# Kernel optimization log

Hardware: AMD Instinct MI355X
Metric: run time of the kernel (lower is better)

## Reference

```python
import jax, jax.numpy as jnp
import numpy as np

T, D = 1024, 2048
H, KH, HD = 16, 4, 128
E, K, I = 8, 2, 2048
EPS = 1e-5
CAP = 30.0          # attn logit softcap and router logit softcap
BASE = 10000.0      # rope theta


def setup_inputs() -> dict:
    key = jax.random.key(0)
    ks = jax.random.split(key, 8)
    s = 0.02
    return {
        "positions": jnp.arange(T, dtype=jnp.int32),
        "hidden_states": jax.random.normal(ks[0], (T, D), jnp.float32),
        "w_qkv": jax.random.normal(ks[1], (D, (H + 2 * KH) * HD), jnp.float32) * s,
        "w_o": jax.random.normal(ks[2], (H * HD, D), jnp.float32) * s,
        "w_gate": jax.random.normal(ks[3], (D, E), jnp.float32) * s,
        "w_gate_up": jax.random.normal(ks[4], (E, D, 2 * I), jnp.float32) * s,
        "w_down": jax.random.normal(ks[5], (E, I, D), jnp.float32) * s,
        "w_pre_attn": 1.0 + 0.01 * jax.random.normal(ks[6], (D,), jnp.float32),
        "w_post_attn": jnp.ones((D,), jnp.float32),
        "w_pre_moe": 1.0 + 0.01 * jax.random.normal(ks[7], (D,), jnp.float32),
        "w_post_moe": jnp.ones((D,), jnp.float32),
    }


def rmsnorm(x, w):
    v = jnp.mean(jnp.square(x), axis=-1, keepdims=True)
    return x * jax.lax.rsqrt(v + EPS) * w


def rope_neox(pos, x):
    # x: [T, nH, HD]; full-head-dim neox-style rotation
    half = HD // 2
    inv = 1.0 / (BASE ** (jnp.arange(half, dtype=jnp.float32) * 2.0 / HD))
    f = pos.astype(jnp.float32)[:, None] * inv            # [T, half]
    cos, sin = jnp.cos(f)[:, None, :], jnp.sin(f)[:, None, :]
    x1, x2 = x[..., :half], x[..., half:]
    return jnp.concatenate([x1 * cos - x2 * sin, x2 * cos + x1 * sin], axis=-1)


def attention(pos, x, w_qkv, w_o):
    qkv = x @ w_qkv
    q, k, v = jnp.split(qkv, [H * HD, (H + KH) * HD], axis=-1)
    q = rope_neox(pos, q.reshape(T, H, HD))
    k = rope_neox(pos, k.reshape(T, KH, HD))
    v = v.reshape(T, KH, HD)
    rep = H // KH                                          # GQA repeat
    k = jnp.repeat(k, rep, axis=1)
    v = jnp.repeat(v, rep, axis=1)
    s = jnp.einsum('qhd,khd->hqk', q, k) * (HD ** -0.5)
    s = CAP * jnp.tanh(s / CAP)                            # tanh logit cap
    causal = pos[:, None] >= pos[None, :]
    s = jnp.where(causal[None], s, -1e30)
    p = jax.nn.softmax(s, axis=-1)
    o = jnp.einsum('hqk,khd->qhd', p, v).reshape(T, H * HD)
    return o @ w_o


def moe(x, w_gate, w_gate_up, w_down):
    logits = x @ w_gate
    logits = CAP * jnp.tanh(logits / CAP)                  # router softcap
    probs = jax.nn.softmax(logits, axis=-1)
    topv, topi = jax.lax.top_k(probs, K)                   # no renorm (Grok1)
    comb = jnp.zeros((T, E), probs.dtype).at[jnp.arange(T)[:, None], topi].set(topv)
    gu = jnp.einsum('td,edf->etf', x, w_gate_up)           # [E,T,2I]
    g, u = jnp.split(gu, 2, axis=-1)
    act = jax.nn.gelu(g, approximate=True) * u             # GeluAndMul(tanh)
    out_e = jnp.einsum('eti,eid->etd', act, w_down)        # [E,T,D]
    return jnp.einsum('etd,te->td', out_e, comb)


def reference(positions, hidden_states, w_qkv, w_o, w_gate, w_gate_up, w_down,
              w_pre_attn, w_post_attn, w_pre_moe, w_post_moe):
    resid = hidden_states
    h = rmsnorm(hidden_states, w_pre_attn)
    a = attention(positions, h, w_qkv, w_o)
    resid = resid + rmsnorm(a, w_post_attn)                # post_attn_norm + add
    h = rmsnorm(resid, w_pre_moe)
    m = moe(h, w_gate, w_gate_up, w_down)
    return resid + rmsnorm(m, w_post_moe)
```

## Files before the change

### kernel.cpp

```cpp
#include <hip/hip_runtime.h>

#define TT 1024
#define DD 2048
#define NH 16
#define NKV 4
#define HDIM 128
#define NE 8
#define NI 2048
#define EPSF 1e-5f

typedef short bf16x8 __attribute__((ext_vector_type(8)));
typedef float f32x4 __attribute__((ext_vector_type(4)));

__device__ __forceinline__ unsigned short f2bf(float x) {
  unsigned u = __float_as_uint(x);
  u += 0x7FFFu + ((u >> 16) & 1u);
  return (unsigned short)(u >> 16);
}
__device__ __forceinline__ float bf2f(unsigned short h) {
  return __uint_as_float((unsigned)h << 16);
}
__device__ __forceinline__ void split2(float a, unsigned short& h,
                                       unsigned short& l) {
  h = f2bf(a);
  l = f2bf(a - bf2f(h));
}

__device__ __forceinline__ float wave_sum(float v) {
#pragma unroll
  for (int m = 32; m >= 1; m >>= 1) v += __shfl_xor(v, m, 64);
  return v;
}
__device__ __forceinline__ float wave_max(float v) {
#pragma unroll
  for (int m = 32; m >= 1; m >>= 1) v = fmaxf(v, __shfl_xor(v, m, 64));
  return v;
}

__device__ __forceinline__ int swz4(int r) { return (r ^ (r >> 2)) & 3; }
__device__ __forceinline__ int swz8(int r) { return (r ^ (r >> 3)) & 7; }

__device__ __forceinline__ void stage32(char* dst, const unsigned short* src,
                                        int rs, int tid) {
#pragma unroll
  for (int j = 0; j < 2; ++j) {
    int idx = tid + j * 256;
    int r = idx >> 2, c = idx & 3;
    bf16x8 v = *(const bf16x8*)(src + r * rs + c * 8);
    *(bf16x8*)(dst + r * 64 + ((c ^ swz4(r)) << 4)) = v;
  }
}
__device__ __forceinline__ void ld_frag(const char* base, int wrow, int l15,
                                        int lg, bf16x8* dst) {
#pragma unroll
  for (int i = 0; i < 4; ++i) {
    int row = wrow + i * 16 + l15;
    dst[i] = *(const bf16x8*)(base + row * 64 + ((lg ^ swz4(row)) << 4));
  }
}
__device__ __forceinline__ void mm16(const bf16x8* xa, const bf16x8* xb,
                                     f32x4 (*acc)[4]) {
#pragma unroll
  for (int mi = 0; mi < 4; ++mi)
#pragma unroll
    for (int ni = 0; ni < 4; ++ni)
      acc[mi][ni] = __builtin_amdgcn_mfma_f32_16x16x32_bf16(
          xa[mi], xb[ni], acc[mi][ni], 0, 0, 0);
}

template <int MODE>
__global__ __launch_bounds__(256) void pgemm3_k(
    const unsigned short* __restrict__ Ah, const unsigned short* __restrict__ Al,
    const unsigned short* __restrict__ Bh, const unsigned short* __restrict__ Bl,
    float* __restrict__ C, int Kh, int lda, int ldb, int ldc, long czs,
    float escale) {
  int z = blockIdx.z;
  int m0 = blockIdx.y * 128, n0 = blockIdx.x * 128;
  int k0 = 0, kend = Kh;
  if (MODE == 0) {
    k0 = z * Kh;
    kend = k0 + Kh;
    C += (long)z * czs;
  } else if (MODE == 1) {
    if (blockIdx.x > blockIdx.y) return;
    Ah += (long)z * TT * lda;
    Al += (long)z * TT * lda;
    Bh += (long)(z >> 2) * TT * ldb;
    Bl += (long)(z >> 2) * TT * ldb;
    C += (long)z * czs;
  } else {
    int head = z >> 2, ch = z & 3;
    int limit = (blockIdx.y + 1) * 128;
    k0 = ch * 256;
    if (k0 >= limit) return;
    kend = k0 + 256 < limit ? k0 + 256 : limit;
    Ah += (long)head * TT * lda;
    Al += (long)head * TT * lda;
    Bh += (long)(head >> 2) * HDIM * ldb;
    Bl += (long)(head >> 2) * HDIM * ldb;
    C += (long)ch * czs + head * HDIM;
  }

  __shared__ __align__(16) char lds[32768];
  int tid = threadIdx.x, lane = tid & 63, wid = tid >> 6;
  int wm = (wid >> 1) * 64, wn = (wid & 1) * 64;
  int l15 = lane & 15, lg = lane >> 4;

  f32x4 acc[4][4];
#pragma unroll
  for (int i = 0; i < 4; ++i)
#pragma unroll
    for (int j = 0; j < 4; ++j) acc[i][j] = {0.f, 0.f, 0.f, 0.f};

  for (int kt = k0; kt < kend; kt += 32) {
    __syncthreads();
    stage32(lds, Ah + (long)m0 * lda + kt, lda, tid);
    stage32(lds + 8192, Al + (long)m0 * lda + kt, lda, tid);
    stage32(lds + 16384, Bh + (long)n0 * ldb + kt, ldb, tid);
    stage32(lds + 24576, Bl + (long)n0 * ldb + kt, ldb, tid);
    __syncthreads();
    bf16x8 fah[4], fal[4], fbh[4], fbl[4];
    ld_frag(lds, wm, l15, lg, fah);
    ld_frag(lds + 16384, wn, l15, lg, fbh);
    mm16(fah, fbh, acc);
    ld_frag(lds + 24576, wn, l15, lg, fbl);
    mm16(fah, fbl, acc);
    ld_frag(lds + 8192, wm, l15, lg, fal);
    mm16(fal, fbh, acc);
  }
#pragma unroll
  for (int mi = 0; mi < 4; ++mi)
#pragma unroll
    for (int ni = 0; ni < 4; ++ni)
#pragma unroll
      for (int rr = 0; rr < 4; ++rr) {
        int ml = m0 + wm + mi * 16 + lg * 4 + rr;
        int col = n0 + wn + ni * 16 + l15;
        float val = acc[mi][ni][rr];
        if (MODE == 1) {
          val *= escale;
          val = 30.f * tanhf(val * (1.f / 30.f));
        }
        C[(long)ml * ldc + col] = val;
      }
}

template <int AMODE, int EP>
__global__ __launch_bounds__(256) void gemm_k(
    const unsigned short* __restrict__ A, const float* __restrict__ Bf,
    float* __restrict__ Cf, int N, int K, int lda, int ldb, int ldc, long bzs,
    const int* __restrict__ cnt, const int* __restrict__ basep,
    const int* __restrict__ tok, const int* __restrict__ slotp,
    const float* __restrict__ wtp, float* __restrict__ slots_out) {
  int z = blockIdx.z;
  Bf += (long)z * bzs;
  int Me = cnt[z], be = basep[z];
  int m0 = blockIdx.y * 128, n0 = blockIdx.x * 128;
  if (m0 >= Me) return;

  __shared__ __align__(16) char lds[32768];
  const int BOFF = 16384;
  int tid = threadIdx.x, lane = tid & 63, wid = tid >> 6;
  int wm = (wid >> 1) * 64, wn = (wid & 1) * 64;
  int l15 = lane & 15, lg = lane >> 4;

  f32x4 acc[4][4];
#pragma unroll
  for (int i = 0; i < 4; ++i)
#pragma unroll
    for (int j = 0; j < 4; ++j) acc[i][j] = {0.f, 0.f, 0.f, 0.f};

  for (int kt = 0; kt < K; kt += 64) {
    __syncthreads();
#pragma unroll
    for (int i = 0; i < 4; ++i) {
      int idx = tid + i * 256;
      int r = idx >> 3, c = idx & 7;
      int gm = m0 + r;
      bf16x8 v = {0, 0, 0, 0, 0, 0, 0, 0};
      bool ok = gm < Me;
      long arow;
      if (AMODE == 1)
        arow = ok ? (long)tok[z * TT + gm] : 0;
      else
        arow = (long)be + gm;
      if (ok) v = *(const bf16x8*)(A + arow * (long)lda + kt + c * 8);
      *(bf16x8*)(lds + r * 128 + ((c ^ swz8(r)) << 4)) = v;
    }
#pragma unroll
    for (int i = 0; i < 4; ++i) {
      int gidx = tid + i * 256;
      int n = gidx & 127, kc = gidx >> 7;
      const float* src = Bf + (long)(kt + kc * 8) * ldb + n0 + n;
      bf16x8 v;
#pragma unroll
      for (int u = 0; u < 8; ++u)
        ((unsigned short*)&v)[u] = f2bf(src[(long)u * ldb]);
      *(bf16x8*)(lds + BOFF + n * 128 + ((kc ^ swz8(n)) << 4)) = v;
    }
    __syncthreads();
#pragma unroll
    for (int s = 0; s < 2; ++s) {
      bf16x8 af[4], bfr[4];
      int slotk = s * 4 + lg;
#pragma unroll
      for (int mi = 0; mi < 4; ++mi) {
        int row = wm + mi * 16 + l15;
        af[mi] =
            *(const bf16x8*)(lds + row * 128 + ((slotk ^ swz8(row)) << 4));
      }
#pragma unroll
      for (int ni = 0; ni < 4; ++ni) {
        int row = wn + ni * 16 + l15;
        bfr[ni] = *(const bf16x8*)(lds + BOFF + row * 128 +
                                   ((slotk ^ swz8(row)) << 4));
      }
      mm16(af, bfr, acc);
    }
  }
#pragma unroll
  for (int mi = 0; mi < 4; ++mi)
#pragma unroll
    for (int ni = 0; ni < 4; ++ni)
#pragma unroll
      for (int rr = 0; rr < 4; ++rr) {
        int ml = m0 + wm + mi * 16 + lg * 4 + rr;
        int col = n0 + wn + ni * 16 + l15;
        float val = acc[mi][ni][rr];
        if (ml < Me) {
          if (EP == 0) {
            Cf[(long)(be + ml) * ldc + col] = val;
          } else {
            int t = tok[z * TT + ml];
            int s = slotp[z * TT + ml];
            float w = wtp[z * TT + ml];
            slots_out[((long)s * TT + t) * DD + col] = val * w;
          }
        }
      }
}

__global__ __launch_bounds__(256) void tsplit_k(const float* __restrict__ W,
                                                unsigned short* __restrict__ Th,
                                                unsigned short* __restrict__ Tl,
                                                int K, int N) {
  __shared__ float lds[64 * 65];
  int n0 = blockIdx.x * 64, k0 = blockIdx.y * 64;
  int tid = threadIdx.x;
#pragma unroll
  for (int i = 0; i < 4; ++i) {
    int idx = tid + i * 256;
    int kr = idx >> 4, cg = idx & 15;
    float4 v = *(const float4*)(W + (long)(k0 + kr) * N + n0 + cg * 4);
    float* p = &lds[kr * 65 + cg * 4];
    p[0] = v.x; p[1] = v.y; p[2] = v.z; p[3] = v.w;
  }
  __syncthreads();
#pragma unroll
  for (int i = 0; i < 2; ++i) {
    int idx = tid + i * 256;
    int n = idx >> 3, kc = idx & 7;
    bf16x8 h8, l8;
#pragma unroll
    for (int u = 0; u < 8; ++u) {
      unsigned short hh, ll;
      split2(lds[(kc * 8 + u) * 65 + n], hh, ll);
      ((unsigned short*)&h8)[u] = hh;
      ((unsigned short*)&l8)[u] = ll;
    }
    long o = (long)(n0 + n) * K + k0 + kc * 8;
    *(bf16x8*)(Th + o) = h8;
    *(bf16x8*)(Tl + o) = l8;
  }
}

__global__ __launch_bounds__(256) void rms_pre_k(const float* __restrict__ x,
                                                 const float* __restrict__ w,
                                                 unsigned short* __restrict__ oh,
                                                 unsigned short* __restrict__ ol) {
  __shared__ float red[4];
  int t = blockIdx.x, tid = threadIdx.x;
  const float* xr = x + (long)t * DD;
  float xv[8];
  float ss = 0.f;
#pragma unroll
  for (int i = 0; i < 8; ++i) {
    float v = xr[tid + i * 256];
    xv[i] = v;
    ss += v * v;
  }
  ss = wave_sum(ss);
  if ((tid & 63) == 0) red[tid >> 6] = ss;
  __syncthreads();
  float r = rsqrtf((red[0] + red[1] + red[2] + red[3]) * (1.f / DD) + EPSF);
#pragma unroll
  for (int i = 0; i < 8; ++i) {
    int d = tid + i * 256;
    split2(xv[i] * r * w[d], oh[(long)t * DD + d], ol[(long)t * DD + d]);
  }
}

__global__ __launch_bounds__(256) void rope_qk_k(
    const int* __restrict__ pos, const float* __restrict__ p0,
    const float* __restrict__ p1, unsigned short* __restrict__ qh,
    unsigned short* __restrict__ ql, unsigned short* __restrict__ kh,
    unsigned short* __restrict__ kl) {
  __shared__ float cs[64], sn[64];
  int t = blockIdx.x, tid = threadIdx.x;
  float pf = (float)pos[t];
  if (tid < 64) {
    float inv = exp2f(-(float)tid * 0.20762050593046015f);
    float f = pf * inv;
    cs[tid] = cosf(f);
    sn[tid] = sinf(f);
  }
  __syncthreads();
  const float* r0 = p0 + (long)t * 3072;
  const float* r1 = p1 + (long)t * 3072;
#pragma unroll
  for (int i = 0; i < 4; ++i) {
    int idx = tid + i * 256;
    int h = idx >> 6, j = idx & 63;
    float x1 = r0[h * HDIM + j] + r1[h * HDIM + j];
    float x2 = r0[h * HDIM + 64 + j] + r1[h * HDIM + 64 + j];
    float c = cs[j], s = sn[j];
    long base = ((long)h * TT + t) * HDIM;
    split2(x1 * c - x2 * s, qh[base + j], ql[base + j]);
    split2(x2 * c + x1 * s, qh[base + 64 + j], ql[base + 64 + j]);
  }
  {
    int k2 = tid >> 6, j = tid & 63;
    float x1 = r0[2048 + k2 * HDIM + j] + r1[2048 + k2 * HDIM + j];
    float x2 = r0[2048 + k2 * HDIM + 64 + j] + r1[2048 + k2 * HDIM + 64 + j];
    float c = cs[j], s = sn[j];
    long base = ((long)k2 * TT + t) * HDIM;
    split2(x1 * c - x2 * s, kh[base + j], kl[base + j]);
    split2(x2 * c + x1 * s, kh[base + 64 + j], kl[base + 64 + j]);
  }
}

__global__ __launch_bounds__(256) void vtrans_k(const float* __restrict__ p0,
                                                const float* __restrict__ p1,
                                                unsigned short* __restrict__ Vh,
                                                unsigned short* __restrict__ Vl) {
  __shared__ float lds[64 * 129];
  int tb = blockIdx.x, kv = blockIdx.y;
  int t0 = tb * 128;
  int tid = threadIdx.x;
#pragma unroll
  for (int dh = 0; dh < 2; ++dh) {
    if (dh) __syncthreads();
#pragma unroll
    for (int i = 0; i < 8; ++i) {
      int fidx = tid + i * 256;
      int t = fidx >> 4, dq = fidx & 15;
      long gi = (long)(t0 + t) * 3072 + 2560 + kv * HDIM + dh * 64 + dq * 4;
      float4 a = *(const float4*)(p0 + gi);
      float4 b = *(const float4*)(p1 + gi);
      lds[(dq * 4 + 0) * 129 + t] = a.x + b.x;
      lds[(dq * 4 + 1) * 129 + t] = a.y + b.y;
      lds[(dq * 4 + 2) * 129 + t] = a.z + b.z;
      lds[(dq * 4 + 3) * 129 + t] = a.w + b.w;
    }
    __syncthreads();
#pragma unroll
    for (int i = 0; i < 4; ++i) {
      int cidx = tid + i * 256;
      int d = cidx >> 4, tc = cidx & 15;
      bf16x8 h8, l8;
#pragma unroll
      for (int u = 0; u < 8; ++u) {
        unsigned short hh, ll;
        split2(lds[d * 129 + tc * 8 + u], hh, ll);
        ((unsigned short*)&h8)[u] = hh;
        ((unsigned short*)&l8)[u] = ll;
      }
      long o = ((long)kv * HDIM + dh * 64 + d) * TT + t0 + tc * 8;
      *(bf16x8*)(Vh + o) = h8;
      *(bf16x8*)(Vl + o) = l8;
    }
  }
}

__global__ __launch_bounds__(256) void softmax_k(const float* __restrict__ S,
                                                 unsigned short* __restrict__ Ph,
                                                 unsigned short* __restrict__ Pl) {
  __shared__ float red[4];
  int i = blockIdx.x, h = blockIdx.y, tid = threadIdx.x;
  int len = i + 1;
  const float* srow = S + ((long)h * TT + i) * TT;
  unsigned short* ph = Ph + ((long)h * TT + i) * TT;
  unsigned short* pl = Pl + ((long)h * TT + i) * TT;
  float m = -1e30f;
  for (int j = tid; j < len; j += 256) m = fmaxf(m, srow[j]);
  m = wave_max(m);
  if ((tid & 63) == 0) red[tid >> 6] = m;
  __syncthreads();
  m = fmaxf(fmaxf(red[0], red[1]), fmaxf(red[2], red[3]));
  __syncthreads();
  float ssum = 0.f;
  for (int j = tid; j < len; j += 256) ssum += expf(srow[j] - m);
  ssum = wave_sum(ssum);
  if ((tid & 63) == 0) red[tid >> 6] = ssum;
  __syncthreads();
  float inv = 1.f / (red[0] + red[1] + red[2] + red[3]);
  for (int j = tid; j < TT; j += 256) {
    float p = (j < len) ? expf(srow[j] - m) * inv : 0.f;
    unsigned short hh, ll;
    split2(p, hh, ll);
    ph[j] = hh;
    pl[j] = ll;
  }
}

__global__ __launch_bounds__(256) void obreduce_k(const float* __restrict__ obp,
                                                  unsigned short* __restrict__ oh,
                                                  unsigned short* __restrict__ ol) {
  int m = blockIdx.x, tid = threadIdx.x;
  int nv = ((m >> 7) >> 1) + 1;
#pragma unroll
  for (int i = 0; i < 8; ++i) {
    int d = tid + i * 256;
    float s = 0.f;
    for (int c = 0; c < nv; ++c) s += obp[(long)c * TT * DD + (long)m * DD + d];
    split2(s, oh[(long)m * DD + d], ol[(long)m * DD + d]);
  }
}

__global__ __launch_bounds__(256) void post_attn_k(
    const float* __restrict__ a0, const float* __restrict__ a1,
    const float* __restrict__ hidden, const float* __restrict__ w_post,
    const float* __restrict__ w_pre2, float* __restrict__ resid1,
    float* __restrict__ h2f, unsigned short* __restrict__ h2b) {
  __shared__ float red[4];
  int t = blockIdx.x, tid = threadIdx.x;
  float av[8];
  float ss = 0.f;
#pragma unroll
  for (int i = 0; i < 8; ++i) {
    long o = (long)t * DD + tid + i * 256;
    float v = a0[o] + a1[o];
    av[i] = v;
    ss += v * v;
  }
  ss = wave_sum(ss);
  if ((tid & 63) == 0) red[tid >> 6] = ss;
  __syncthreads();
  float r1 = rsqrtf((red[0] + red[1] + red[2] + red[3]) * (1.f / DD) + EPSF);
  __syncthreads();
  float rv[8];
  float ss2 = 0.f;
#pragma unroll
  for (int i = 0; i < 8; ++i) {
    int d = tid + i * 256;
    float v = hidden[(long)t * DD + d] + av[i] * r1 * w_post[d];
    rv[i] = v;
    resid1[(long)t * DD + d] = v;
    ss2 += v * v;
  }
  ss2 = wave_sum(ss2);
  if ((tid & 63) == 0) red[tid >> 6] = ss2;
  __syncthreads();
  float r2 = rsqrtf((red[0] + red[1] + red[2] + red[3]) * (1.f / DD) + EPSF);
#pragma unroll
  for (int i = 0; i < 8; ++i) {
    int d = tid + i * 256;
    float hv = rv[i] * r2 * w_pre2[d];
    h2f[(long)t * DD + d] = hv;
    h2b[(long)t * DD + d] = f2bf(hv);
  }
}

__global__ __launch_bounds__(256) void gate_k(const float* __restrict__ h2f,
                                              const float* __restrict__ wg,
                                              int* cnt, int* tok, int* slotp,
                                              float* wtp) {
  __shared__ float red[4][8];
  int t = blockIdx.x, tid = threadIdx.x;
  float a[8] = {0, 0, 0, 0, 0, 0, 0, 0};
  const float* x = h2f + (long)t * DD;
  for (int d = tid; d < DD; d += 256) {
    float xv = x[d];
    const float* wr = wg + d * 8;
#pragma unroll
    for (int e = 0; e < 8; ++e) a[e] += xv * wr[e];
  }
#pragma unroll
  for (int e = 0; e < 8; ++e) a[e] = wave_sum(a[e]);
  if ((tid & 63) == 0) {
#pragma unroll
    for (int e = 0; e < 8; ++e) red[tid >> 6][e] = a[e];
  }
  __syncthreads();
  if (tid == 0) {
    float l[8], p[8];
    float m = -1e30f;
    for (int e = 0; e < 8; ++e) {
      float v = red[0][e] + red[1][e] + red[2][e] + red[3][e];
      v = 30.f * tanhf(v * (1.f / 30.f));
      l[e] = v;
      m = fmaxf(m, v);
    }
    float s = 0.f;
    for (int e = 0; e < 8; ++e) { p[e] = expf(l[e] - m); s += p[e]; }
    for (int e = 0; e < 8; ++e) p[e] /= s;
    int i1 = 0;
    for (int e = 1; e < 8; ++e) if (p[e] > p[i1]) i1 = e;
    int i2 = (i1 == 0) ? 1 : 0;
    for (int e = 0; e < 8; ++e) if (e != i1 && p[e] > p[i2]) i2 = e;
    int q1 = atomicAdd(&cnt[i1], 1);
    tok[i1 * TT + q1] = t; slotp[i1 * TT + q1] = 0; wtp[i1 * TT + q1] = p[i1];
    int q2 = atomicAdd(&cnt[i2], 1);
    tok[i2 * TT + q2] = t; slotp[i2 * TT + q2] = 1; wtp[i2 * TT + q2] = p[i2];
  }
}

__global__ void scan_k(const int* __restrict__ cnt, int* __restrict__ basep) {
  if (threadIdx.x == 0) {
    int s = 0;
    for (int e = 0; e < NE; ++e) { basep[e] = s; s += cnt[e]; }
    basep[NE] = s;
  }
}

__global__ __launch_bounds__(256) void act_k(const float* __restrict__ gu,
                                             unsigned short* __restrict__ actb) {
  long a = blockIdx.x;
  const float* g = gu + a * (2 * NI);
  for (int i = threadIdx.x; i < NI; i += 256) {
    float gg = g[i], uu = g[i + NI];
    float c = gg + 0.044715f * gg * gg * gg;
    float act = 0.5f * gg * (1.f + tanhf(0.7978845608028654f * c));
    actb[a * NI + i] = f2bf(act * uu);
  }
}

__global__ __launch_bounds__(256) void final_k(const float* __restrict__ resid1,
                                               const float* __restrict__ slots,
                                               const float* __restrict__ w2,
                                               float* __restrict__ out) {
  __shared__ float red[4];
  int t = blockIdx.x, tid = threadIdx.x;
  float mv[8];
  float ss = 0.f;
#pragma unroll
  for (int i = 0; i < 8; ++i) {
    int d = tid + i * 256;
    float v = slots[(long)t * DD + d] + slots[((long)TT + t) * DD + d];
    mv[i] = v;
    ss += v * v;
  }
  ss = wave_sum(ss);
  if ((tid & 63) == 0) red[tid >> 6] = ss;
  __syncthreads();
  float r = rsqrtf((red[0] + red[1] + red[2] + red[3]) * (1.f / DD) + EPSF);
#pragma unroll
  for (int i = 0; i < 8; ++i) {
    int d = tid + i * 256;
    out[(long)t * DD + d] = resid1[(long)t * DD + d] + mv[i] * r * w2[d];
  }
}

__global__ void sentinel_k(float* out) { out[threadIdx.x] = 12345.0f; }

extern "C" void kernel_launch(void* const* d_in, const int* in_sizes, int n_in,
                              void* d_out, int out_size, void* d_ws,
                              size_t ws_size, hipStream_t stream) {
  const int* pos = (const int*)d_in[0];
  const float* hidden = (const float*)d_in[1];
  const float* w_qkv = (const float*)d_in[2];
  const float* w_o = (const float*)d_in[3];
  const float* w_gate = (const float*)d_in[4];
  const float* w_gu = (const float*)d_in[5];
  const float* w_down = (const float*)d_in[6];
  const float* w_pre_attn = (const float*)d_in[7];
  const float* w_post_attn = (const float*)d_in[8];
  const float* w_pre_moe = (const float*)d_in[9];
  const float* w_post_moe = (const float*)d_in[10];
  float* out = (float*)d_out;

  char* ws = (char*)d_ws;
  size_t off = 0;
  auto alloc = [&](size_t bytes) {
    char* p = ws + off;
    off += (bytes + 255) & ~(size_t)255;
    return p;
  };
  typedef unsigned short u16;
  u16* h1h = (u16*)alloc((size_t)TT * DD * 2);
  u16* h1l = (u16*)alloc((size_t)TT * DD * 2);
  u16* wqkvTh = (u16*)alloc((size_t)3072 * DD * 2);
  u16* wqkvTl = (u16*)alloc((size_t)3072 * DD * 2);
  float* qkvp = (float*)alloc((size_t)2 * TT * 3072 * 4);
  u16* qh_ = (u16*)alloc((size_t)NH * TT * HDIM * 2);
  u16* ql_ = (u16*)alloc((size_t)NH * TT * HDIM * 2);
  u16* kh_ = (u16*)alloc((size_t)NKV * TT * HDIM * 2);
  u16* kl_ = (u16*)alloc((size_t)NKV * TT * HDIM * 2);
  u16* vth = (u16*)alloc((size_t)NKV * HDIM * TT * 2);
  u16* vtl = (u16*)alloc((size_t)NKV * HDIM * TT * 2);
  float* S = (float*)alloc((size_t)NH * TT * TT * 4);
  u16* Ph = (u16*)alloc((size_t)NH * TT * TT * 2);
  u16* Pl = (u16*)alloc((size_t)NH * TT * TT * 2);
  float* obp = (float*)alloc((size_t)4 * TT * DD * 4);
  u16* obh = (u16*)alloc((size_t)TT * DD * 2);
  u16* obl = (u16*)alloc((size_t)TT * DD * 2);
  u16* woTh = (u16*)alloc((size_t)DD * DD * 2);
  u16* woTl = (u16*)alloc((size_t)DD * DD * 2);
  float* attnp = (float*)alloc((size_t)2 * TT * DD * 4);
  float* resid1 = (float*)alloc((size_t)TT * DD * 4);
  float* h2f = (float*)alloc((size_t)TT * DD * 4);
  u16* h2b = (u16*)alloc((size_t)TT * DD * 2);
  int* cnt = (int*)alloc(NE * 4);
  int* basep = (int*)alloc((NE + 1) * 4);
  int* tok = (int*)alloc((size_t)NE * TT * 4);
  int* slotp = (int*)alloc((size_t)NE * TT * 4);
  float* wtp = (float*)alloc((size_t)NE * TT * 4);
  float* gu = (float*)alloc((size_t)2 * TT * 2 * NI * 4);
  u16* actb = (u16*)alloc((size_t)2 * TT * NI * 2);
  float* slots = (float*)alloc((size_t)2 * TT * DD * 4);

  if (off > ws_size) {
    sentinel_k<<<1, 256, 0, stream>>>(out);
    return;
  }

  hipMemsetAsync(cnt, 0, NE * 4, stream);
  dim3 blk(256);

  rms_pre_k<<<TT, blk, 0, stream>>>(hidden, w_pre_attn, h1h, h1l);
  tsplit_k<<<dim3(3072 / 64, DD / 64), blk, 0, stream>>>(w_qkv, wqkvTh, wqkvTl,
                                                         DD, 3072);
  tsplit_k<<<dim3(DD / 64, DD / 64), blk, 0, stream>>>(w_o, woTh, woTl, DD, DD);

  pgemm3_k<0><<<dim3(3072 / 128, TT / 128, 2), blk, 0, stream>>>(
      h1h, h1l, wqkvTh, wqkvTl, qkvp, 1024, DD, DD, 3072, (long)TT * 3072, 0.f);

  rope_qk_k<<<TT, blk, 0, stream>>>(pos, qkvp, qkvp + (size_t)TT * 3072, qh_,
                                    ql_, kh_, kl_);
  vtrans_k<<<dim3(8, NKV), blk, 0, stream>>>(qkvp, qkvp + (size_t)TT * 3072,
                                             vth, vtl);

  pgemm3_k<1><<<dim3(TT / 128, TT / 128, NH), blk, 0, stream>>>(
      qh_, ql_, kh_, kl_, S, HDIM, HDIM, HDIM, TT, (long)TT * TT,
      0.08838834764831845f);

  softmax_k<<<dim3(TT, NH), blk, 0, stream>>>(S, Ph, Pl);

  pgemm3_k<2><<<dim3(1, TT / 128, NH * 4), blk, 0, stream>>>(
      Ph, Pl, vth, vtl, obp, 256, TT, TT, DD, (long)TT * DD, 0.f);
  obreduce_k<<<TT, blk, 0, stream>>>(obp, obh, obl);

  pgemm3_k<0><<<dim3(DD / 128, TT / 128, 2), blk, 0, stream>>>(
      obh, obl, woTh, woTl, attnp, 1024, DD, DD, DD, (long)TT * DD, 0.f);

  post_attn_k<<<TT, blk, 0, stream>>>(attnp, attnp + (size_t)TT * DD, hidden,
                                      w_post_attn, w_pre_moe, resid1, h2f, h2b);
  gate_k<<<TT, blk, 0, stream>>>(h2f, w_gate, cnt, tok, slotp, wtp);
  scan_k<<<1, 64, 0, stream>>>(cnt, basep);

  gemm_k<1, 0><<<dim3(2 * NI / 128, TT / 128, NE), blk, 0, stream>>>(
      h2b, w_gu, gu, 2 * NI, DD, DD, 2 * NI, 2 * NI, (long)DD * 2 * NI, cnt,
      basep, tok, nullptr, nullptr, nullptr);

  act_k<<<2 * TT, blk, 0, stream>>>(gu, actb);

  gemm_k<2, 3><<<dim3(DD / 128, TT / 128, NE), blk, 0, stream>>>(
      actb, w_down, nullptr, DD, NI, NI, DD, DD, (long)NI * DD, cnt, basep,
      tok, slotp, wtp, slots);

  final_k<<<TT, blk, 0, stream>>>(resid1, slots, w_post_moe, out);
}
```

Measured before the change: 536.8 us.

## Split-K projections four ways, enlarge MoE GEMM tiles, trim softmax writes

```diff
diff --git a/kernel.cpp b/kernel.cpp
--- a/kernel.cpp
+++ b/kernel.cpp
@@ -8,6 +8,7 @@
 #define NE 8
 #define NI 2048
 #define EPSF 1e-5f
+#define NP 4
 
 typedef short bf16x8 __attribute__((ext_vector_type(8)));
 typedef float f32x4 __attribute__((ext_vector_type(4)));
@@ -146,7 +147,7 @@
 }
 
 template <int AMODE, int EP>
-__global__ __launch_bounds__(256) void gemm_k(
+__global__ __launch_bounds__(512) void gemm_k(
     const unsigned short* __restrict__ A, const float* __restrict__ Bf,
     float* __restrict__ Cf, int N, int K, int lda, int ldb, int ldc, long bzs,
     const int* __restrict__ cnt, const int* __restrict__ basep,
@@ -155,11 +156,11 @@
   int z = blockIdx.z;
   Bf += (long)z * bzs;
   int Me = cnt[z], be = basep[z];
-  int m0 = blockIdx.y * 128, n0 = blockIdx.x * 128;
+  int m0 = blockIdx.y * 256, n0 = blockIdx.x * 128;
   if (m0 >= Me) return;
 
-  __shared__ __align__(16) char lds[32768];
-  const int BOFF = 16384;
+  __shared__ __align__(16) char lds[49152];
+  const int BOFF = 32768;
   int tid = threadIdx.x, lane = tid & 63, wid = tid >> 6;
   int wm = (wid >> 1) * 64, wn = (wid & 1) * 64;
   int l15 = lane & 15, lg = lane >> 4;
@@ -174,7 +175,7 @@
     __syncthreads();
 #pragma unroll
     for (int i = 0; i < 4; ++i) {
-      int idx = tid + i * 256;
+      int idx = tid + i * 512;
       int r = idx >> 3, c = idx & 7;
       int gm = m0 + r;
       bf16x8 v = {0, 0, 0, 0, 0, 0, 0, 0};
@@ -188,8 +189,8 @@
       *(bf16x8*)(lds + r * 128 + ((c ^ swz8(r)) << 4)) = v;
     }
 #pragma unroll
-    for (int i = 0; i < 4; ++i) {
-      int gidx = tid + i * 256;
+    for (int i = 0; i < 2; ++i) {
+      int gidx = tid + i * 512;
       int n = gidx & 127, kc = gidx >> 7;
       const float* src = Bf + (long)(kt + kc * 8) * ldb + n0 + n;
       bf16x8 v;
@@ -301,10 +302,9 @@
 }
 
 __global__ __launch_bounds__(256) void rope_qk_k(
-    const int* __restrict__ pos, const float* __restrict__ p0,
-    const float* __restrict__ p1, unsigned short* __restrict__ qh,
-    unsigned short* __restrict__ ql, unsigned short* __restrict__ kh,
-    unsigned short* __restrict__ kl) {
+    const int* __restrict__ pos, const float* __restrict__ qp,
+    unsigned short* __restrict__ qh, unsigned short* __restrict__ ql,
+    unsigned short* __restrict__ kh, unsigned short* __restrict__ kl) {
   __shared__ float cs[64], sn[64];
   int t = blockIdx.x, tid = threadIdx.x;
   float pf = (float)pos[t];
@@ -315,14 +315,18 @@
     sn[tid] = sinf(f);
   }
   __syncthreads();
-  const float* r0 = p0 + (long)t * 3072;
-  const float* r1 = p1 + (long)t * 3072;
+  const float* row = qp + (long)t * 3072;
+  const long PS = (long)TT * 3072;
 #pragma unroll
   for (int i = 0; i < 4; ++i) {
     int idx = tid + i * 256;
     int h = idx >> 6, j = idx & 63;
-    float x1 = r0[h * HDIM + j] + r1[h * HDIM + j];
-    float x2 = r0[h * HDIM + 64 + j] + r1[h * HDIM + 64 + j];
+    float x1 = 0.f, x2 = 0.f;
+#pragma unroll
+    for (int p = 0; p < NP; ++p) {
+      x1 += row[p * PS + h * HDIM + j];
+      x2 += row[p * PS + h * HDIM + 64 + j];
+    }
     float c = cs[j], s = sn[j];
     long base = ((long)h * TT + t) * HDIM;
     split2(x1 * c - x2 * s, qh[base + j], ql[base + j]);
@@ -330,8 +334,12 @@
   }
   {
     int k2 = tid >> 6, j = tid & 63;
-    float x1 = r0[2048 + k2 * HDIM + j] + r1[2048 + k2 * HDIM + j];
-    float x2 = r0[2048 + k2 * HDIM + 64 + j] + r1[2048 + k2 * HDIM + 64 + j];
+    float x1 = 0.f, x2 = 0.f;
+#pragma unroll
+    for (int p = 0; p < NP; ++p) {
+      x1 += row[p * PS + 2048 + k2 * HDIM + j];
+      x2 += row[p * PS + 2048 + k2 * HDIM + 64 + j];
+    }
     float c = cs[j], s = sn[j];
     long base = ((long)k2 * TT + t) * HDIM;
     split2(x1 * c - x2 * s, kh[base + j], kl[base + j]);
@@ -339,14 +347,14 @@
   }
 }
 
-__global__ __launch_bounds__(256) void vtrans_k(const float* __restrict__ p0,
-                                                const float* __restrict__ p1,
+__global__ __launch_bounds__(256) void vtrans_k(const float* __restrict__ qp,
                                                 unsigned short* __restrict__ Vh,
                                                 unsigned short* __restrict__ Vl) {
   __shared__ float lds[64 * 129];
   int tb = blockIdx.x, kv = blockIdx.y;
   int t0 = tb * 128;
   int tid = threadIdx.x;
+  const long PS = (long)TT * 3072;
 #pragma unroll
   for (int dh = 0; dh < 2; ++dh) {
     if (dh) __syncthreads();
@@ -355,12 +363,16 @@
       int fidx = tid + i * 256;
       int t = fidx >> 4, dq = fidx & 15;
       long gi = (long)(t0 + t) * 3072 + 2560 + kv * HDIM + dh * 64 + dq * 4;
-      float4 a = *(const float4*)(p0 + gi);
-      float4 b = *(const float4*)(p1 + gi);
-      lds[(dq * 4 + 0) * 129 + t] = a.x + b.x;
-      lds[(dq * 4 + 1) * 129 + t] = a.y + b.y;
-      lds[(dq * 4 + 2) * 129 + t] = a.z + b.z;
-      lds[(dq * 4 + 3) * 129 + t] = a.w + b.w;
+      float4 a = *(const float4*)(qp + gi);
+#pragma unroll
+      for (int p = 1; p < NP; ++p) {
+        float4 b = *(const float4*)(qp + p * PS + gi);
+        a.x += b.x; a.y += b.y; a.z += b.z; a.w += b.w;
+      }
+      lds[(dq * 4 + 0) * 129 + t] = a.x;
+      lds[(dq * 4 + 1) * 129 + t] = a.y;
+      lds[(dq * 4 + 2) * 129 + t] = a.z;
+      lds[(dq * 4 + 3) * 129 + t] = a.w;
     }
     __syncthreads();
 #pragma unroll
@@ -388,6 +400,7 @@
   __shared__ float red[4];
   int i = blockIdx.x, h = blockIdx.y, tid = threadIdx.x;
   int len = i + 1;
+  int wlimit = ((i >> 7) + 1) << 7;
   const float* srow = S + ((long)h * TT + i) * TT;
   unsigned short* ph = Ph + ((long)h * TT + i) * TT;
   unsigned short* pl = Pl + ((long)h * TT + i) * TT;
@@ -404,7 +417,7 @@
   if ((tid & 63) == 0) red[tid >> 6] = ssum;
   __syncthreads();
   float inv = 1.f / (red[0] + red[1] + red[2] + red[3]);
-  for (int j = tid; j < TT; j += 256) {
+  for (int j = tid; j < wlimit; j += 256) {
     float p = (j < len) ? expf(srow[j] - m) * inv : 0.f;
     unsigned short hh, ll;
     split2(p, hh, ll);
@@ -428,18 +441,21 @@
 }
 
 __global__ __launch_bounds__(256) void post_attn_k(
-    const float* __restrict__ a0, const float* __restrict__ a1,
-    const float* __restrict__ hidden, const float* __restrict__ w_post,
-    const float* __restrict__ w_pre2, float* __restrict__ resid1,
-    float* __restrict__ h2f, unsigned short* __restrict__ h2b) {
+    const float* __restrict__ ap, const float* __restrict__ hidden,
+    const float* __restrict__ w_post, const float* __restrict__ w_pre2,
+    float* __restrict__ resid1, float* __restrict__ h2f,
+    unsigned short* __restrict__ h2b) {
   __shared__ float red[4];
   int t = blockIdx.x, tid = threadIdx.x;
+  const long PS = (long)TT * DD;
   float av[8];
   float ss = 0.f;
 #pragma unroll
   for (int i = 0; i < 8; ++i) {
     long o = (long)t * DD + tid + i * 256;
-    float v = a0[o] + a1[o];
+    float v = 0.f;
+#pragma unroll
+    for (int p = 0; p < NP; ++p) v += ap[p * PS + o];
     av[i] = v;
     ss += v * v;
   }
@@ -591,7 +607,7 @@
   u16* h1l = (u16*)alloc((size_t)TT * DD * 2);
   u16* wqkvTh = (u16*)alloc((size_t)3072 * DD * 2);
   u16* wqkvTl = (u16*)alloc((size_t)3072 * DD * 2);
-  float* qkvp = (float*)alloc((size_t)2 * TT * 3072 * 4);
+  float* qkvp = (float*)alloc((size_t)NP * TT * 3072 * 4);
   u16* qh_ = (u16*)alloc((size_t)NH * TT * HDIM * 2);
   u16* ql_ = (u16*)alloc((size_t)NH * TT * HDIM * 2);
   u16* kh_ = (u16*)alloc((size_t)NKV * TT * HDIM * 2);
@@ -606,7 +622,7 @@
   u16* obl = (u16*)alloc((size_t)TT * DD * 2);
   u16* woTh = (u16*)alloc((size_t)DD * DD * 2);
   u16* woTl = (u16*)alloc((size_t)DD * DD * 2);
-  float* attnp = (float*)alloc((size_t)2 * TT * DD * 4);
+  float* attnp = (float*)alloc((size_t)NP * TT * DD * 4);
   float* resid1 = (float*)alloc((size_t)TT * DD * 4);
   float* h2f = (float*)alloc((size_t)TT * DD * 4);
   u16* h2b = (u16*)alloc((size_t)TT * DD * 2);
@@ -632,13 +648,12 @@
                                                          DD, 3072);
   tsplit_k<<<dim3(DD / 64, DD / 64), blk, 0, stream>>>(w_o, woTh, woTl, DD, DD);
 
-  pgemm3_k<0><<<dim3(3072 / 128, TT / 128, 2), blk, 0, stream>>>(
-      h1h, h1l, wqkvTh, wqkvTl, qkvp, 1024, DD, DD, 3072, (long)TT * 3072, 0.f);
-
-  rope_qk_k<<<TT, blk, 0, stream>>>(pos, qkvp, qkvp + (size_t)TT * 3072, qh_,
-                                    ql_, kh_, kl_);
-  vtrans_k<<<dim3(8, NKV), blk, 0, stream>>>(qkvp, qkvp + (size_t)TT * 3072,
-                                             vth, vtl);
+  pgemm3_k<0><<<dim3(3072 / 128, TT / 128, NP), blk, 0, stream>>>(
+      h1h, h1l, wqkvTh, wqkvTl, qkvp, DD / NP, DD, DD, 3072, (long)TT * 3072,
+      0.f);
+
+  rope_qk_k<<<TT, blk, 0, stream>>>(pos, qkvp, qh_, ql_, kh_, kl_);
+  vtrans_k<<<dim3(8, NKV), blk, 0, stream>>>(qkvp, vth, vtl);
 
   pgemm3_k<1><<<dim3(TT / 128, TT / 128, NH), blk, 0, stream>>>(
       qh_, ql_, kh_, kl_, S, HDIM, HDIM, HDIM, TT, (long)TT * TT,
@@ -650,21 +665,21 @@
       Ph, Pl, vth, vtl, obp, 256, TT, TT, DD, (long)TT * DD, 0.f);
   obreduce_k<<<TT, blk, 0, stream>>>(obp, obh, obl);
 
-  pgemm3_k<0><<<dim3(DD / 128, TT / 128, 2), blk, 0, stream>>>(
-      obh, obl, woTh, woTl, attnp, 1024, DD, DD, DD, (long)TT * DD, 0.f);
-
-  post_attn_k<<<TT, blk, 0, stream>>>(attnp, attnp + (size_t)TT * DD, hidden,
-                                      w_post_attn, w_pre_moe, resid1, h2f, h2b);
+  pgemm3_k<0><<<dim3(DD / 128, TT / 128, NP), blk, 0, stream>>>(
+      obh, obl, woTh, woTl, attnp, DD / NP, DD, DD, DD, (long)TT * DD, 0.f);
+
+  post_attn_k<<<TT, blk, 0, stream>>>(attnp, hidden, w_post_attn, w_pre_moe,
+                                      resid1, h2f, h2b);
   gate_k<<<TT, blk, 0, stream>>>(h2f, w_gate, cnt, tok, slotp, wtp);
   scan_k<<<1, 64, 0, stream>>>(cnt, basep);
 
-  gemm_k<1, 0><<<dim3(2 * NI / 128, TT / 128, NE), blk, 0, stream>>>(
+  gemm_k<1, 0><<<dim3(2 * NI / 128, TT / 256, NE), dim3(512), 0, stream>>>(
       h2b, w_gu, gu, 2 * NI, DD, DD, 2 * NI, 2 * NI, (long)DD * 2 * NI, cnt,
       basep, tok, nullptr, nullptr, nullptr);
 
   act_k<<<2 * TT, blk, 0, stream>>>(gu, actb);
 
-  gemm_k<2, 3><<<dim3(DD / 128, TT / 128, NE), blk, 0, stream>>>(
+  gemm_k<2, 3><<<dim3(DD / 128, TT / 256, NE), dim3(512), 0, stream>>>(
       actb, w_down, nullptr, DD, NI, NI, DD, DD, (long)NI * DD, cnt, basep,
       tok, slotp, wtp, slots);
 
```

New measurement: 624.0 us. 1.16x slower.
